# Kernel optimization log

Hardware: AMD Instinct MI355X
Metric: run time of the kernel (lower is better)

## Reference

```python
import jax, jax.numpy as jnp
import numpy as np

B, D, L, E, R = 16384, 2048, 3, 8, 64


def setup_inputs() -> dict:
    key = jax.random.key(0)
    k1, k2, k3, k4 = jax.random.split(key, 4)
    scale = 1.0 / np.sqrt(D)  # ~ PyTorch Linear default init scale
    X0 = jax.random.normal(k1, (B, D), dtype=jnp.float32)
    U = jax.random.normal(k2, (L, E, R, D), dtype=jnp.float32) * scale
    V = jax.random.normal(k3, (L, E, R, D), dtype=jnp.float32) * scale
    Wg = jax.random.normal(k4, (L, E, D), dtype=jnp.float32) * scale
    bg = jnp.zeros((L, E), dtype=jnp.float32)
    return {"X0": X0, "U": U, "V": V, "Wg": Wg, "bg": bg}


def reference(X0, U, V, Wg, bg):
    # X0: (B, D); U, V: (L, E, R, D); Wg: (L, E, D); bg: (L, E)
    Xi = X0
    num_layers = U.shape[0]
    for l in range(num_layers):  # small fixed layer count
        gate = jax.nn.softmax(jnp.einsum('bd,ed->be', Xi, Wg[l]) + bg[l], axis=1)  # (B, E)
        Uo = jnp.einsum('bd,erd->ber', Xi, U[l])  # (B, E, R)
        Vo = jnp.einsum('bd,erd->ber', Xi, V[l])  # (B, E, R)
        expert_out = jnp.sum(Uo * Vo, axis=2)     # (B, E) low-rank bilinear forms
        xw = jnp.sum(expert_out * gate, axis=1, keepdims=True)  # (B, 1)
        Xi = Xi + X0 * xw  # residual cross update (dropout=0, eval mode)
    return Xi
```

## Files before the change

### kernel.cpp

```cpp
#include <hip/hip_runtime.h>
#include <hip/hip_bf16.h>

#define BDIM 16384
#define DDIM 2048
#define LNUM 3
#define ENUM 8
#define NP 24

#define BM 256
#define BK 32

typedef _Float16 f16x8 __attribute__((ext_vector_type(8)));
typedef _Float16 f16x4 __attribute__((ext_vector_type(4)));
typedef float f32x4 __attribute__((ext_vector_type(4)));

__global__ void cvt_w_kernel(const float* __restrict__ U, const float* __restrict__ V,
                             _Float16* __restrict__ Wh) {
    size_t f = (size_t)blockIdx.x * blockDim.x + threadIdx.x;
    size_t elem = f * 4;
    int d   = (int)(elem & (DDIM - 1));
    int row = (int)((elem >> 11) & 127);
    int p   = (int)(elem >> 18);
    const float* src = (row < 64)
        ? (U + ((size_t)(p * 64 + row) * DDIM + d))
        : (V + ((size_t)(p * 64 + (row - 64)) * DDIM + d));
    float4 v = *(const float4*)src;
    f16x4 h = { (_Float16)v.x, (_Float16)v.y, (_Float16)v.z, (_Float16)v.w };
    ((f16x4*)Wh)[f] = h;
}

__global__ __launch_bounds__(256, 4) void gate_kernel(
    const float* __restrict__ X0, const float* __restrict__ Wg,
    float* __restrict__ G, _Float16* __restrict__ X0h) {
    __shared__ float Wgs[NP * 256];
    const int tid = (int)threadIdx.x;
    const int rq  = tid >> 3;
    const int q   = tid & 7;
    const int r0  = blockIdx.x * 64 + rq;
    const int r1  = r0 + 32;

    float acc[2][NP];
#pragma unroll
    for (int r = 0; r < 2; ++r)
#pragma unroll
        for (int j = 0; j < NP; ++j) acc[r][j] = 0.f;

    const float4* x0p = (const float4*)(X0 + (size_t)r0 * DDIM);
    const float4* x1p = (const float4*)(X0 + (size_t)r1 * DDIM);
    f16x4* h0p = (f16x4*)(X0h + (size_t)r0 * DDIM);
    f16x4* h1p = (f16x4*)(X0h + (size_t)r1 * DDIM);

    for (int k0 = 0; k0 < DDIM; k0 += 256) {
        __syncthreads();
#pragma unroll
        for (int t = tid; t < NP * 64; t += 256)
            ((float4*)Wgs)[t] =
                ((const float4*)Wg)[(size_t)(t >> 6) * (DDIM / 4) + (k0 >> 2) + (t & 63)];
        __syncthreads();
#pragma unroll 2
        for (int i = 0; i < 8; ++i) {
            int f4 = i * 8 + q;
            int gc = (k0 >> 2) + f4;
            float4 x0 = x0p[gc];
            float4 x1 = x1p[gc];
            f16x4 h0 = { (_Float16)x0.x, (_Float16)x0.y, (_Float16)x0.z, (_Float16)x0.w };
            f16x4 h1 = { (_Float16)x1.x, (_Float16)x1.y, (_Float16)x1.z, (_Float16)x1.w };
            h0p[gc] = h0;
            h1p[gc] = h1;
#pragma unroll
            for (int j = 0; j < NP; ++j) {
                float4 w = ((const float4*)(Wgs + j * 256))[f4];
                acc[0][j] += x0.x * w.x + x0.y * w.y + x0.z * w.z + x0.w * w.w;
                acc[1][j] += x1.x * w.x + x1.y * w.y + x1.z * w.z + x1.w * w.w;
            }
        }
    }
#pragma unroll
    for (int r = 0; r < 2; ++r)
#pragma unroll
        for (int j = 0; j < NP; ++j) {
            float v = acc[r][j];
            v += __shfl_xor(v, 1);
            v += __shfl_xor(v, 2);
            v += __shfl_xor(v, 4);
            if (q == 0) G[(size_t)j * BDIM + (r == 0 ? r0 : r1)] = v;
        }
}

__global__ __launch_bounds__(256, 2) void gemm_t_kernel(
    const _Float16* __restrict__ Ah,
    const _Float16* __restrict__ Bh,
    float* __restrict__ T)
{
    const int p    = blockIdx.y;
    const int m0   = blockIdx.x * BM;
    const int tid  = (int)threadIdx.x;
    const int wave = tid >> 6;
    const int lane = tid & 63;
    const int mlane = lane & 15;
    const int quad  = lane >> 4;

    __shared__ _Float16 As[BM * BK];
    __shared__ _Float16 Bs[128 * BK];

    const _Float16* Bp = Bh + (size_t)p * 128 * DDIM;

    f32x4 acc[4][8];
#pragma unroll
    for (int i = 0; i < 4; ++i)
#pragma unroll
        for (int j = 0; j < 8; ++j) acc[i][j] = (f32x4){0.f, 0.f, 0.f, 0.f};

    const int srow = lane >> 2;
    const int scol = ((lane & 3) ^ ((lane >> 3) & 3)) * 8;
    const int sw   = (mlane >> 1) & 3;

    for (int k0 = 0; k0 < DDIM; k0 += BK) {
        __syncthreads();
#pragma unroll
        for (int q = 0; q < 4; ++q) {
            int r16 = wave * 64 + q * 16;
            const _Float16* ga = Ah + (size_t)(m0 + r16 + srow) * DDIM + k0 + scol;
            __builtin_amdgcn_global_load_lds(
                (const __attribute__((address_space(1))) void*)ga,
                (__attribute__((address_space(3))) void*)&As[r16 * BK], 16, 0, 0);
        }
#pragma unroll
        for (int q = 0; q < 2; ++q) {
            int r16 = wave * 32 + q * 16;
            const _Float16* gb = Bp + (size_t)(r16 + srow) * DDIM + k0 + scol;
            __builtin_amdgcn_global_load_lds(
                (const __attribute__((address_space(1))) void*)gb,
                (__attribute__((address_space(3))) void*)&Bs[r16 * BK], 16, 0, 0);
        }
        __syncthreads();

        f16x8 aF[4], bF[8];
#pragma unroll
        for (int mi = 0; mi < 4; ++mi)
            aF[mi] = *(const f16x8*)&As[(wave * 64 + mi * 16 + mlane) * BK + ((quad ^ sw) * 8)];
#pragma unroll
        for (int ni = 0; ni < 8; ++ni)
            bF[ni] = *(const f16x8*)&Bs[(ni * 16 + mlane) * BK + ((quad ^ sw) * 8)];
#pragma unroll
        for (int mi = 0; mi < 4; ++mi)
#pragma unroll
            for (int ni = 0; ni < 8; ++ni)
                acc[mi][ni] = __builtin_amdgcn_mfma_f32_16x16x32_f16(
                    aF[mi], bF[ni], acc[mi][ni], 0, 0, 0);
    }

#pragma unroll
    for (int mi = 0; mi < 4; ++mi) {
#pragma unroll
        for (int j = 0; j < 4; ++j) {
            float tp = 0.f;
#pragma unroll
            for (int ni = 0; ni < 4; ++ni)
                tp += acc[mi][ni][j] * acc[mi][ni + 4][j];
            tp += __shfl_xor(tp, 1);
            tp += __shfl_xor(tp, 2);
            tp += __shfl_xor(tp, 4);
            tp += __shfl_xor(tp, 8);
            if (mlane == 0) {
                int m = wave * 64 + mi * 16 + quad * 4 + j;
                T[(size_t)p * BDIM + (m0 + m)] = tp;
            }
        }
    }
}

__global__ void epilogue_kernel(const _Float16* __restrict__ X0h,
                                const float* __restrict__ T,
                                const float* __restrict__ G,
                                const float* __restrict__ bg,
                                float* __restrict__ out) {
    __shared__ float s_sh[16];
    const int b0 = blockIdx.x * 16;
    const int tid = (int)threadIdx.x;
    if (tid < 16) {
        int b = b0 + tid;
        float s = 1.f;
#pragma unroll
        for (int l = 0; l < LNUM; ++l) {
            float logit[ENUM];
            float mx = -1e30f;
#pragma unroll
            for (int e = 0; e < ENUM; ++e) {
                int j = l * ENUM + e;
                float g = s * G[(size_t)j * BDIM + b] + bg[j];
                logit[e] = g;
                mx = fmaxf(mx, g);
            }
            float den = 0.f, num = 0.f;
            float s2 = s * s;
#pragma unroll
            for (int e = 0; e < ENUM; ++e) {
                int j = l * ENUM + e;
                float w = __expf(logit[e] - mx);
                den += w;
                num += w * (s2 * T[(size_t)j * BDIM + b]);
            }
            s += num / den;
        }
        s_sh[tid] = s;
    }
    __syncthreads();
    const int nf4 = DDIM / 4;
    for (int idx = tid; idx < 16 * nf4; idx += 256) {
        int r = idx >> 9;
        int c = idx & (nf4 - 1);
        float s = s_sh[r];
        f16x4 h = ((const f16x4*)(X0h + (size_t)(b0 + r) * DDIM))[c];
        float4 x = { s * (float)h[0], s * (float)h[1], s * (float)h[2], s * (float)h[3] };
        ((float4*)(out + (size_t)(b0 + r) * DDIM))[c] = x;
    }
}

extern "C" void kernel_launch(void* const* d_in, const int* in_sizes, int n_in,
                              void* d_out, int out_size, void* d_ws, size_t ws_size,
                              hipStream_t stream) {
    const float* X0 = (const float*)d_in[0];
    const float* U  = (const float*)d_in[1];
    const float* V  = (const float*)d_in[2];
    const float* Wg = (const float*)d_in[3];
    const float* bg = (const float*)d_in[4];
    float* out = (float*)d_out;

    char* ws = (char*)d_ws;
    _Float16* X0h = (_Float16*)ws;
    _Float16* Wh  = (_Float16*)(ws + 67108864ull);
    float* T      = (float*)(ws + 67108864ull + 12582912ull);
    float* G      = (float*)(ws + 67108864ull + 12582912ull + 1572864ull);

    cvt_w_kernel<<<dim3((NP * 128 * DDIM / 4) / 256), dim3(256), 0, stream>>>(U, V, Wh);
    gate_kernel<<<dim3(BDIM / 64), dim3(256), 0, stream>>>(X0, Wg, G, X0h);
    gemm_t_kernel<<<dim3(BDIM / BM, NP), dim3(256), 0, stream>>>(X0h, Wh, T);
    epilogue_kernel<<<dim3(BDIM / 16), dim3(256), 0, stream>>>(X0h, T, G, bg, out);
}
```

Measured before the change: 542.0 us.

## Pre-swizzle fp16 operands into MFMA fragment layout and use 32x32 MFMA

The X0 and weight fp16 copies are now written in a fragment-major layout matching the 32x32x16 MFMA operand order. This lets the GEMM load A fragments straight from global memory into registers and load B through a double-buffered LDS stage with no swizzle. BK rises to 64, and the next K-step's loads are prefetched while the current one computes. The gate kernel and epilogue are adapted to write and read the new layout, which gives up row-contiguous global accesses and adds register pressure from the larger accumulators and prefetched fragments.

```diff
diff --git a/kernel.cpp b/kernel.cpp
--- a/kernel.cpp
+++ b/kernel.cpp
@@ -8,47 +8,48 @@
 #define NP 24
 
 #define BM 256
-#define BK 32
+#define BK 64
+#define NKIT (DDIM / BK)
 
 typedef _Float16 f16x8 __attribute__((ext_vector_type(8)));
 typedef _Float16 f16x4 __attribute__((ext_vector_type(4)));
-typedef float f32x4 __attribute__((ext_vector_type(4)));
+typedef float f32x16 __attribute__((ext_vector_type(16)));
+
 
 __global__ void cvt_w_kernel(const float* __restrict__ U, const float* __restrict__ V,
-                             _Float16* __restrict__ Wh) {
-    size_t f = (size_t)blockIdx.x * blockDim.x + threadIdx.x;
-    size_t elem = f * 4;
-    int d   = (int)(elem & (DDIM - 1));
-    int row = (int)((elem >> 11) & 127);
-    int p   = (int)(elem >> 18);
-    const float* src = (row < 64)
-        ? (U + ((size_t)(p * 64 + row) * DDIM + d))
-        : (V + ((size_t)(p * 64 + (row - 64)) * DDIM + d));
-    float4 v = *(const float4*)src;
-    f16x4 h = { (_Float16)v.x, (_Float16)v.y, (_Float16)v.z, (_Float16)v.w };
-    ((f16x4*)Wh)[f] = h;
-}
-
-__global__ __launch_bounds__(256, 4) void gate_kernel(
+                             _Float16* __restrict__ Whf) {
+    int idx = blockIdx.x * 256 + threadIdx.x;
+    int f8     = idx & 255;
+    int row128 = (idx >> 8) & 127;
+    int p      = idx >> 15;
+    const float* src = (row128 < 64)
+        ? (U + ((size_t)(p * 64 + row128) * DDIM + f8 * 8))
+        : (V + ((size_t)(p * 64 + (row128 - 64)) * DDIM + f8 * 8));
+    float4 a = ((const float4*)src)[0];
+    float4 b = ((const float4*)src)[1];
+    f16x8 h = { (_Float16)a.x, (_Float16)a.y, (_Float16)a.z, (_Float16)a.w,
+                (_Float16)b.x, (_Float16)b.y, (_Float16)b.z, (_Float16)b.w };
+    int gn = row128 >> 5, col = row128 & 31;
+    int kw = f8 >> 1, khalf = f8 & 1;
+    size_t C = ((size_t)((p * 4 + gn) * 128 + kw)) * 64 + khalf * 32 + col;
+    ((f16x8*)Whf)[C] = h;
+}
+
+__global__ __launch_bounds__(256, 2) void gate_kernel(
     const float* __restrict__ X0, const float* __restrict__ Wg,
-    float* __restrict__ G, _Float16* __restrict__ X0h) {
+    float* __restrict__ G, _Float16* __restrict__ X0f) {
     __shared__ float Wgs[NP * 256];
     const int tid = (int)threadIdx.x;
     const int rq  = tid >> 3;
     const int q   = tid & 7;
-    const int r0  = blockIdx.x * 64 + rq;
-    const int r1  = r0 + 32;
-
-    float acc[2][NP];
-#pragma unroll
-    for (int r = 0; r < 2; ++r)
-#pragma unroll
-        for (int j = 0; j < NP; ++j) acc[r][j] = 0.f;
-
-    const float4* x0p = (const float4*)(X0 + (size_t)r0 * DDIM);
-    const float4* x1p = (const float4*)(X0 + (size_t)r1 * DDIM);
-    f16x4* h0p = (f16x4*)(X0h + (size_t)r0 * DDIM);
-    f16x4* h1p = (f16x4*)(X0h + (size_t)r1 * DDIM);
+    const int r0  = blockIdx.x * 32 + rq;
+    const int g32 = blockIdx.x;
+
+    float acc[NP];
+#pragma unroll
+    for (int j = 0; j < NP; ++j) acc[j] = 0.f;
+
+    const float4* xp = (const float4*)(X0 + (size_t)r0 * DDIM);
 
     for (int k0 = 0; k0 < DDIM; k0 += 256) {
         __syncthreads();
@@ -58,38 +59,38 @@
                 ((const float4*)Wg)[(size_t)(t >> 6) * (DDIM / 4) + (k0 >> 2) + (t & 63)];
         __syncthreads();
 #pragma unroll 2
-        for (int i = 0; i < 8; ++i) {
-            int f4 = i * 8 + q;
-            int gc = (k0 >> 2) + f4;
-            float4 x0 = x0p[gc];
-            float4 x1 = x1p[gc];
-            f16x4 h0 = { (_Float16)x0.x, (_Float16)x0.y, (_Float16)x0.z, (_Float16)x0.w };
-            f16x4 h1 = { (_Float16)x1.x, (_Float16)x1.y, (_Float16)x1.z, (_Float16)x1.w };
-            h0p[gc] = h0;
-            h1p[gc] = h1;
+        for (int i = 0; i < 4; ++i) {
+            int f8 = i * 8 + q;
+            int gcf4 = (k0 >> 2) + f8 * 2;
+            float4 xa = xp[gcf4];
+            float4 xb = xp[gcf4 + 1];
+            f16x8 h = { (_Float16)xa.x, (_Float16)xa.y, (_Float16)xa.z, (_Float16)xa.w,
+                        (_Float16)xb.x, (_Float16)xb.y, (_Float16)xb.z, (_Float16)xb.w };
+            int kw = (k0 >> 4) + (f8 >> 1);
+            int khalf = f8 & 1;
+            ((f16x8*)X0f)[((size_t)(g32 * 128 + kw)) * 64 + khalf * 32 + rq] = h;
 #pragma unroll
             for (int j = 0; j < NP; ++j) {
-                float4 w = ((const float4*)(Wgs + j * 256))[f4];
-                acc[0][j] += x0.x * w.x + x0.y * w.y + x0.z * w.z + x0.w * w.w;
-                acc[1][j] += x1.x * w.x + x1.y * w.y + x1.z * w.z + x1.w * w.w;
-            }
-        }
-    }
-#pragma unroll
-    for (int r = 0; r < 2; ++r)
-#pragma unroll
-        for (int j = 0; j < NP; ++j) {
-            float v = acc[r][j];
-            v += __shfl_xor(v, 1);
-            v += __shfl_xor(v, 2);
-            v += __shfl_xor(v, 4);
-            if (q == 0) G[(size_t)j * BDIM + (r == 0 ? r0 : r1)] = v;
-        }
+                float4 wa = ((const float4*)(Wgs + j * 256))[f8 * 2];
+                float4 wb = ((const float4*)(Wgs + j * 256))[f8 * 2 + 1];
+                acc[j] += xa.x * wa.x + xa.y * wa.y + xa.z * wa.z + xa.w * wa.w
+                        + xb.x * wb.x + xb.y * wb.y + xb.z * wb.z + xb.w * wb.w;
+            }
+        }
+    }
+#pragma unroll
+    for (int j = 0; j < NP; ++j) {
+        float v = acc[j];
+        v += __shfl_xor(v, 1);
+        v += __shfl_xor(v, 2);
+        v += __shfl_xor(v, 4);
+        if (q == 0) G[(size_t)j * BDIM + r0] = v;
+    }
 }
 
 __global__ __launch_bounds__(256, 2) void gemm_t_kernel(
-    const _Float16* __restrict__ Ah,
-    const _Float16* __restrict__ Bh,
+    const _Float16* __restrict__ X0f,
+    const _Float16* __restrict__ Whf,
     float* __restrict__ T)
 {
     const int p    = blockIdx.y;
@@ -97,80 +98,91 @@
     const int tid  = (int)threadIdx.x;
     const int wave = tid >> 6;
     const int lane = tid & 63;
-    const int mlane = lane & 15;
-    const int quad  = lane >> 4;
-
-    __shared__ _Float16 As[BM * BK];
-    __shared__ _Float16 Bs[128 * BK];
-
-    const _Float16* Bp = Bh + (size_t)p * 128 * DDIM;
-
-    f32x4 acc[4][8];
-#pragma unroll
-    for (int i = 0; i < 4; ++i)
-#pragma unroll
-        for (int j = 0; j < 8; ++j) acc[i][j] = (f32x4){0.f, 0.f, 0.f, 0.f};
-
-    const int srow = lane >> 2;
-    const int scol = ((lane & 3) ^ ((lane >> 3) & 3)) * 8;
-    const int sw   = (mlane >> 1) & 3;
-
-    for (int k0 = 0; k0 < DDIM; k0 += BK) {
+
+    __shared__ _Float16 Bs[2 * 16 * 512];
+
+    const int g32b = (m0 >> 5) + wave * 2;
+
+    f32x16 acc[2][4];
+#pragma unroll
+    for (int i = 0; i < 2; ++i)
+#pragma unroll
+        for (int j = 0; j < 4; ++j) acc[i][j] = (f32x16)(0.f);
+
+    f16x8 aF[2][8];
+
+#pragma unroll
+    for (int kw = 0; kw < 4; ++kw) {
+        const _Float16* gb = Whf + (((size_t)((p * 4 + wave) * 128 + kw)) * 64 + lane) * 8;
+        __builtin_amdgcn_global_load_lds(
+            (const __attribute__((address_space(1))) void*)gb,
+            (__attribute__((address_space(3))) void*)&Bs[(wave * 4 + kw) * 512], 16, 0, 0);
+    }
+#pragma unroll
+    for (int mt = 0; mt < 2; ++mt)
+#pragma unroll
+        for (int kw = 0; kw < 4; ++kw)
+            aF[0][mt * 4 + kw] = *(const f16x8*)(
+                X0f + (((size_t)((g32b + mt) * 128 + kw)) * 64 + lane) * 8);
+    __syncthreads();
+
+#pragma unroll 2
+    for (int it = 0; it < NKIT; ++it) {
+        const int cur = it & 1, nxt = cur ^ 1;
+        if (it != NKIT - 1) {
+            const int kwn = (it + 1) * 4;
+#pragma unroll
+            for (int kw = 0; kw < 4; ++kw) {
+                const _Float16* gb =
+                    Whf + (((size_t)((p * 4 + wave) * 128 + kwn + kw)) * 64 + lane) * 8;
+                __builtin_amdgcn_global_load_lds(
+                    (const __attribute__((address_space(1))) void*)gb,
+                    (__attribute__((address_space(3))) void*)&Bs[(nxt * 16 + wave * 4 + kw) * 512],
+                    16, 0, 0);
+            }
+#pragma unroll
+            for (int mt = 0; mt < 2; ++mt)
+#pragma unroll
+                for (int kw = 0; kw < 4; ++kw)
+                    aF[nxt][mt * 4 + kw] = *(const f16x8*)(
+                        X0f + (((size_t)((g32b + mt) * 128 + kwn + kw)) * 64 + lane) * 8);
+        }
+#pragma unroll
+        for (int kw = 0; kw < 4; ++kw) {
+            f16x8 bF[4];
+#pragma unroll
+            for (int gn = 0; gn < 4; ++gn)
+                bF[gn] = *(const f16x8*)&Bs[((cur * 16 + gn * 4 + kw) * 64 + lane) * 8];
+#pragma unroll
+            for (int mt = 0; mt < 2; ++mt)
+#pragma unroll
+                for (int gn = 0; gn < 4; ++gn)
+                    acc[mt][gn] = __builtin_amdgcn_mfma_f32_32x32x16_f16(
+                        aF[cur][mt * 4 + kw], bF[gn], acc[mt][gn], 0, 0, 0);
+        }
         __syncthreads();
-#pragma unroll
-        for (int q = 0; q < 4; ++q) {
-            int r16 = wave * 64 + q * 16;
-            const _Float16* ga = Ah + (size_t)(m0 + r16 + srow) * DDIM + k0 + scol;
-            __builtin_amdgcn_global_load_lds(
-                (const __attribute__((address_space(1))) void*)ga,
-                (__attribute__((address_space(3))) void*)&As[r16 * BK], 16, 0, 0);
-        }
-#pragma unroll
-        for (int q = 0; q < 2; ++q) {
-            int r16 = wave * 32 + q * 16;
-            const _Float16* gb = Bp + (size_t)(r16 + srow) * DDIM + k0 + scol;
-            __builtin_amdgcn_global_load_lds(
-                (const __attribute__((address_space(1))) void*)gb,
-                (__attribute__((address_space(3))) void*)&Bs[r16 * BK], 16, 0, 0);
-        }
-        __syncthreads();
-
-        f16x8 aF[4], bF[8];
-#pragma unroll
-        for (int mi = 0; mi < 4; ++mi)
-            aF[mi] = *(const f16x8*)&As[(wave * 64 + mi * 16 + mlane) * BK + ((quad ^ sw) * 8)];
-#pragma unroll
-        for (int ni = 0; ni < 8; ++ni)
-            bF[ni] = *(const f16x8*)&Bs[(ni * 16 + mlane) * BK + ((quad ^ sw) * 8)];
-#pragma unroll
-        for (int mi = 0; mi < 4; ++mi)
-#pragma unroll
-            for (int ni = 0; ni < 8; ++ni)
-                acc[mi][ni] = __builtin_amdgcn_mfma_f32_16x16x32_f16(
-                    aF[mi], bF[ni], acc[mi][ni], 0, 0, 0);
-    }
-
-#pragma unroll
-    for (int mi = 0; mi < 4; ++mi) {
-#pragma unroll
-        for (int j = 0; j < 4; ++j) {
-            float tp = 0.f;
-#pragma unroll
-            for (int ni = 0; ni < 4; ++ni)
-                tp += acc[mi][ni][j] * acc[mi][ni + 4][j];
+    }
+
+#pragma unroll
+    for (int mt = 0; mt < 2; ++mt) {
+#pragma unroll
+        for (int reg = 0; reg < 16; ++reg) {
+            float tp = acc[mt][0][reg] * acc[mt][2][reg]
+                     + acc[mt][1][reg] * acc[mt][3][reg];
             tp += __shfl_xor(tp, 1);
             tp += __shfl_xor(tp, 2);
             tp += __shfl_xor(tp, 4);
             tp += __shfl_xor(tp, 8);
-            if (mlane == 0) {
-                int m = wave * 64 + mi * 16 + quad * 4 + j;
-                T[(size_t)p * BDIM + (m0 + m)] = tp;
-            }
-        }
-    }
-}
-
-__global__ void epilogue_kernel(const _Float16* __restrict__ X0h,
+            tp += __shfl_xor(tp, 16);
+            if ((lane & 31) == 0) {
+                int row = (reg & 3) + 8 * (reg >> 2) + 4 * (lane >> 5);
+                T[(size_t)p * BDIM + m0 + wave * 64 + mt * 32 + row] = tp;
+            }
+        }
+    }
+}
+
+__global__ void epilogue_kernel(const _Float16* __restrict__ X0f,
                                 const float* __restrict__ T,
                                 const float* __restrict__ G,
                                 const float* __restrict__ bg,
@@ -206,14 +218,18 @@
         s_sh[tid] = s;
     }
     __syncthreads();
-    const int nf4 = DDIM / 4;
-    for (int idx = tid; idx < 16 * nf4; idx += 256) {
-        int r = idx >> 9;
-        int c = idx & (nf4 - 1);
+    for (int idx = tid; idx < 16 * 256; idx += 256) {
+        int r = idx >> 8;
+        int c = idx & 255;
+        int rg = b0 + r;
         float s = s_sh[r];
-        f16x4 h = ((const f16x4*)(X0h + (size_t)(b0 + r) * DDIM))[c];
-        float4 x = { s * (float)h[0], s * (float)h[1], s * (float)h[2], s * (float)h[3] };
-        ((float4*)(out + (size_t)(b0 + r) * DDIM))[c] = x;
+        f16x8 h = ((const f16x8*)X0f)[((size_t)((rg >> 5) * 128 + (c >> 1))) * 64
+                                      + (c & 1) * 32 + (rg & 31)];
+        float4 o0 = { s * (float)h[0], s * (float)h[1], s * (float)h[2], s * (float)h[3] };
+        float4 o1 = { s * (float)h[4], s * (float)h[5], s * (float)h[6], s * (float)h[7] };
+        float4* op = (float4*)(out + (size_t)rg * DDIM + c * 8);
+        op[0] = o0;
+        op[1] = o1;
     }
 }
 
@@ -228,13 +244,13 @@
     float* out = (float*)d_out;
 
     char* ws = (char*)d_ws;
-    _Float16* X0h = (_Float16*)ws;
-    _Float16* Wh  = (_Float16*)(ws + 67108864ull);
+    _Float16* X0f = (_Float16*)ws;
+    _Float16* Whf = (_Float16*)(ws + 67108864ull);
     float* T      = (float*)(ws + 67108864ull + 12582912ull);
     float* G      = (float*)(ws + 67108864ull + 12582912ull + 1572864ull);
 
-    cvt_w_kernel<<<dim3((NP * 128 * DDIM / 4) / 256), dim3(256), 0, stream>>>(U, V, Wh);
-    gate_kernel<<<dim3(BDIM / 64), dim3(256), 0, stream>>>(X0, Wg, G, X0h);
-    gemm_t_kernel<<<dim3(BDIM / BM, NP), dim3(256), 0, stream>>>(X0h, Wh, T);
-    epilogue_kernel<<<dim3(BDIM / 16), dim3(256), 0, stream>>>(X0h, T, G, bg, out);
-}
+    cvt_w_kernel<<<dim3(NP * 128 * 256 / 256), dim3(256), 0, stream>>>(U, V, Whf);
+    gate_kernel<<<dim3(BDIM / 32), dim3(256), 0, stream>>>(X0, Wg, G, X0f);
+    gemm_t_kernel<<<dim3(BDIM / BM, NP), dim3(256), 0, stream>>>(X0f, Whf, T);
+    epilogue_kernel<<<dim3(BDIM / 16), dim3(256), 0, stream>>>(X0f, T, G, bg, out);
+}
```

Measured after the change: 549.7 us. No clear change (+1.4%).
